# Kernel optimization log

Hardware: AMD Instinct MI355X
Metric: run time of the kernel (lower is better)

Reference implementation:

```python
import jax, jax.numpy as jnp
import numpy as np
from jax.scipy.stats import norm as jnorm

B, S, D, H, E, K, FF = 8, 256, 1024, 16, 4, 2, 4096
HD = D // H
NOISE_EPS = 0.01
LOSS_COEF = 0.01
EPS_FILL = float(np.finfo(float).eps)


def _ln(x, g, b):
    m = x.mean(-1, keepdims=True)
    v = x.var(-1, keepdims=True)
    return (x - m) * jax.lax.rsqrt(v + 1e-5) * g + b


def setup_inputs() -> dict:
    key = jax.random.key(0)
    ks = jax.random.split(key, 16)
    r = lambda i, shape, s=1.0: jax.random.normal(ks[i], shape, dtype=jnp.float32) * s
    return {
        "x": r(0, (B, S, D)),
        "e_outputs": r(1, (B, 64, D)),            # unused (is_lm=True) but part of signature
        "noise": r(2, (B, E)),                     # the randn_like(clean_logits) draw
        "w_gate": r(3, (D, E), 0.02),
        "w_noise": r(4, (D, E), 0.02),
        "Wq": r(5, (E, D, D), 0.02),
        "Wk": r(6, (E, D, D), 0.02),
        "Wv": r(7, (E, D, D), 0.02),
        "Wo": r(8, (E, D, D), 0.02),
        "W1": r(9, (E, D, FF), 0.02),
        "b1": jnp.zeros((E, FF), jnp.float32),
        "W2": r(10, (E, FF, D), 0.02),
        "b2": jnp.zeros((E, D), jnp.float32),
        "g1": jnp.ones((E, D), jnp.float32),
        "be1": jnp.zeros((E, D), jnp.float32),
        "g2": jnp.ones((E, D), jnp.float32),
        "be2": jnp.zeros((E, D), jnp.float32),
        "trg_mask": jnp.tril(jnp.ones((S, S), dtype=bool))[None, None],  # causal [1,1,S,S]
        "src_mask": jnp.ones((1, 1, 1, 64), dtype=bool),                 # unused (is_lm=True)
    }


def _cv_squared(v):
    # torch .var() is unbiased (ddof=1)
    return v.var(ddof=1) / (v.mean() ** 2 + 1e-10)


def reference(x, e_outputs, noise, w_gate, w_noise, Wq, Wk, Wv, Wo, W1, b1, W2, b2,
              g1, be1, g2, be2, trg_mask, src_mask):
    b, s, d = x.shape
    # ---- noisy top-k gating (per sample, on the sequence-sum) ----
    xs = x.sum(axis=1)                                   # [B, D]
    clean = xs @ w_gate                                  # [B, E]
    raw_noise = xs @ w_noise                             # [B, E]
    stddev = jax.nn.softplus(raw_noise) + NOISE_EPS      # train=True -> *1.0
    noisy = clean + noise * stddev                       # logits
    top_logits, top_idx = jax.lax.top_k(noisy, K + 1)    # [B, K+1]
    topk_gates = jax.nn.softmax(top_logits[:, :K], axis=1)
    gates = jnp.zeros_like(noisy).at[jnp.arange(b)[:, None], top_idx[:, :K]].set(topk_gates)
    # load: prob each expert's clean logit lands in the noisy top-k
    thr_in = top_logits[:, K:K + 1]                      # (k+1)-th noisy value
    thr_out = top_logits[:, K - 1:K]                     # k-th noisy value
    is_in = noisy > thr_in
    prob = jnp.where(is_in,
                     jnorm.cdf((clean - thr_in) / stddev),
                     jnorm.cdf((clean - thr_out) / stddev))
    load = prob.sum(0)                                   # [E]
    importance = gates.sum(0)                            # [E]
    loss = (_cv_squared(importance) + _cv_squared(load)) * LOSS_COEF

    # ---- experts: standard decoder layer (self-attn + FFN), is_lm -> no cross-attn ----
    neg = jnp.asarray(-1e9, x.dtype)
    scale = 1.0 / np.sqrt(HD)

    def expert(p):
        wq, wk, wv, wo, w1, bb1, w2, bb2, gg1, bbe1, gg2, bbe2 = p
        q = (x @ wq).reshape(b, s, H, HD)
        k_ = (x @ wk).reshape(b, s, H, HD)
        v = (x @ wv).reshape(b, s, H, HD)
        scores = jnp.einsum('bqhd,bkhd->bhqk', q, k_) * scale
        scores = jnp.where(trg_mask, scores, neg)
        attn = jax.nn.softmax(scores, axis=-1)
        o = jnp.einsum('bhqk,bkhd->bqhd', attn, v).reshape(b, s, d) @ wo
        h = _ln(x + o, gg1, bbe1)
        ff = jax.nn.relu(h @ w1 + bb1) @ w2 + bb2
        return _ln(h + ff, gg2, bbe2)

    outs = jax.vmap(expert)((Wq, Wk, Wv, Wo, W1, b1, W2, b2, g1, be1, g2, be2))  # [E,B,S,D]

    # ---- combine: scatter-add of gate-weighted expert outputs (dense equivalent) ----
    y = jnp.einsum('be,ebsd->bsd', gates, outs)
    y = jnp.where(y == 0, jnp.asarray(EPS_FILL, y.dtype), y)
    return y, loss
```

## Files before the change

### kernel.cpp

```cpp
#include <hip/hip_runtime.h>
#include <hip/hip_bf16.h>

typedef __bf16 bf16;
typedef __attribute__((ext_vector_type(4))) __bf16 bf16x4;
typedef __attribute__((ext_vector_type(8))) __bf16 bf16x8;
typedef __attribute__((ext_vector_type(4))) float floatx4;

constexpr int CB = 8, CS = 256, CD = 1024, CH = 16, CE = 4, CFF = 4096, CHD = 64;
constexpr long long DD  = 1048576;
constexpr long long DFF = 4194304;
constexpr long long BSD = 2097152;
constexpr long long PSD = 4194304;

constexpr size_t OFF_PART = 0;
constexpr size_t OFF_CLEAN= 262144;
constexpr size_t OFF_RAW  = 262272;
constexpr size_t OFF_GATES= 262400;
constexpr size_t OFF_EACT = 262528;
constexpr size_t OFF_PBE  = 262592;
constexpr size_t OFF_BP   = 262656;
constexpr size_t OFF_XBF  = 263168;
constexpr size_t OFF_WT   = OFF_XBF + (size_t)BSD*2;
constexpr size_t OFF_W1T  = OFF_WT  + (size_t)16*DD*2;
constexpr size_t OFF_W2T  = OFF_W1T + (size_t)4*DFF*2;
constexpr size_t OFF_QKV  = OFF_W2T + (size_t)4*DFF*2;
constexpr size_t OFF_AO   = OFF_QKV + (size_t)3*PSD*2;
constexpr size_t OFF_F1   = OFF_QKV;
constexpr size_t OFF_PB   = OFF_AO  + (size_t)PSD*2;
constexpr size_t OFF_VT   = OFF_PB;
constexpr size_t OFF_H    = OFF_PB  + (size_t)2*PSD*4;
constexpr size_t OFF_HBF  = OFF_H   + (size_t)PSD*4;

__global__ __launch_bounds__(256)
void cvt_xsum(const float* __restrict__ x, bf16* __restrict__ xbf, float* __restrict__ part) {
  int blk = blockIdx.x;
  int b = blk >> 3, ch = blk & 7;
  int t = threadIdx.x;
  float s0 = 0.f, s1 = 0.f, s2 = 0.f, s3 = 0.f;
  long long base4 = ((long long)(b*CS + ch*32))*CD / 4;
#pragma unroll 4
  for (int r = 0; r < 32; ++r) {
    long long i4 = base4 + (long long)r*(CD/4) + t;
    float4 v = ((const float4*)x)[i4];
    bf16x4 o; o[0] = (bf16)v.x; o[1] = (bf16)v.y; o[2] = (bf16)v.z; o[3] = (bf16)v.w;
    ((bf16x4*)xbf)[i4] = o;
    s0 += v.x; s1 += v.y; s2 += v.z; s3 += v.w;
  }
  float4 sv; sv.x = s0; sv.y = s1; sv.z = s2; sv.w = s3;
  ((float4*)(part + (long long)blk*CD))[t] = sv;
}

__global__ __launch_bounds__(256)
void gate_dots(const float* __restrict__ part, const float* __restrict__ wg,
               const float* __restrict__ wn, float* __restrict__ clean, float* __restrict__ raw) {
  int p = blockIdx.x, b = p >> 2, e = p & 3;
  int t = threadIdx.x;
  float s1 = 0.f, s2 = 0.f;
  for (int d = t; d < CD; d += 256) {
    float xv = 0.f;
#pragma unroll
    for (int c = 0; c < 8; ++c) xv += part[(long long)(b*8 + c)*CD + d];
    s1 += xv * wg[d*CE + e];
    s2 += xv * wn[d*CE + e];
  }
  for (int off = 32; off; off >>= 1) { s1 += __shfl_xor(s1, off); s2 += __shfl_xor(s2, off); }
  __shared__ float r1[4], r2[4];
  int lane = t & 63, w = t >> 6;
  if (lane == 0) { r1[w] = s1; r2[w] = s2; }
  __syncthreads();
  if (t == 0) { clean[p] = r1[0]+r1[1]+r1[2]+r1[3]; raw[p] = r2[0]+r2[1]+r2[2]+r2[3]; }
}

__global__ void gating_kernel(const float* __restrict__ clean, const float* __restrict__ raw,
                              const float* __restrict__ noise, float* __restrict__ gates,
                              int* __restrict__ eact, int* __restrict__ pairBE,
                              int* __restrict__ batchPair, float* __restrict__ loss_out) {
  if (threadIdx.x != 0) return;
  float imp[CE] = {0,0,0,0}, load[CE] = {0,0,0,0};
  int act[CE] = {0,0,0,0};
  for (int b = 0; b < CB; ++b) {
    float cl[CE], sd[CE], ny[CE];
    for (int e = 0; e < CE; ++e) {
      cl[e] = clean[b*CE + e];
      float rw = raw[b*CE + e];
      float sp = fmaxf(rw, 0.f) + log1pf(expf(-fabsf(rw)));
      sd[e] = sp + 0.01f;
      ny[e] = cl[e] + noise[b*CE + e]*sd[e];
    }
    int idx[CE] = {0,1,2,3};
    for (int a = 0; a < 3; ++a) {
      int best = a;
      for (int c = a + 1; c < 4; ++c) if (ny[idx[c]] > ny[idx[best]]) best = c;
      int tt = idx[a]; idx[a] = idx[best]; idx[best] = tt;
    }
    float l0 = ny[idx[0]], l1 = ny[idx[1]], l2 = ny[idx[2]];
    float e1 = expf(l1 - l0);
    float g0 = 1.f/(1.f + e1), g1v = e1/(1.f + e1);
    for (int e = 0; e < CE; ++e) gates[b*CE + e] = 0.f;
    gates[b*CE + idx[0]] = g0; gates[b*CE + idx[1]] = g1v;
    imp[idx[0]] += g0; imp[idx[1]] += g1v;
    act[idx[0]] = 1; act[idx[1]] = 1;
    for (int e = 0; e < CE; ++e) {
      bool is_in = ny[e] > l2;
      float thr = is_in ? l2 : l1;
      float zz = (cl[e] - thr) / sd[e];
      load[e] += 0.5f * erfcf(-zz * 0.70710678118654752440f);
    }
  }
  int pe2p[CB][CE];
  int pc = 0;
  for (int e = 0; e < CE; ++e)
    for (int b = 0; b < CB; ++b)
      if (gates[b*CE + e] != 0.f) { pairBE[pc] = b | (e << 8); pe2p[b][e] = pc; ++pc; }
  for (int b = 0; b < CB; ++b) {
    int s = 0;
    for (int e = 0; e < CE; ++e)
      if (gates[b*CE + e] != 0.f) batchPair[2*b + (s++)] = pe2p[b][e];
  }
  float m1 = 0.f, m2 = 0.f;
  for (int e = 0; e < CE; ++e) { m1 += imp[e]; m2 += load[e]; }
  m1 *= 0.25f; m2 *= 0.25f;
  float v1 = 0.f, v2 = 0.f;
  for (int e = 0; e < CE; ++e) { float d1 = imp[e]-m1, d2 = load[e]-m2; v1 += d1*d1; v2 += d2*d2; }
  v1 *= (1.f/3.f); v2 *= (1.f/3.f);
  loss_out[0] = 0.01f * (v1/(m1*m1 + 1e-10f) + v2/(m2*m2 + 1e-10f));
  for (int e = 0; e < CE; ++e) eact[e] = act[e];
}

__global__ __launch_bounds__(256)
void transcvt_all(const float* __restrict__ Wq, const float* __restrict__ Wk,
                  const float* __restrict__ Wv, const float* __restrict__ Wo,
                  const float* __restrict__ W1, const float* __restrict__ W2,
                  bf16* __restrict__ wT, bf16* __restrict__ w1T, bf16* __restrict__ w2T,
                  const int* __restrict__ eact) {
  int z = blockIdx.x;
  const float* src; bf16* d; int rows, cols, tk, tn, e;
  if (z < 4096) {
    int m = z >> 8, tt = z & 255; e = m >> 2; int which = m & 3;
    src = ((which == 0) ? Wq : (which == 1) ? Wk : (which == 2) ? Wv : Wo) + (long long)e*DD;
    d = wT + (long long)m*DD; rows = 1024; cols = 1024;
    tk = tt >> 4; tn = tt & 15;
  } else if (z < 8192) {
    int z2 = z - 4096; e = z2 >> 10; int tt = z2 & 1023;
    src = W1 + (long long)e*DFF; d = w1T + (long long)e*DFF;
    rows = 1024; cols = 4096; tk = tt >> 6; tn = tt & 63;
  } else {
    int z3 = z - 8192; e = z3 >> 10; int tt = z3 & 1023;
    src = W2 + (long long)e*DFF; d = w2T + (long long)e*DFF;
    rows = 4096; cols = 1024; tk = tt >> 4; tn = tt & 15;
  }
  if (eact[e] == 0) return;
  __shared__ float tile[64][65];
  int t = threadIdx.x;
  int k0 = tk*64, n0 = tn*64;
#pragma unroll
  for (int i = 0; i < 4; ++i) {
    int id = i*256 + t; int r = id >> 4, c4 = id & 15;
    float4 v = *(const float4*)&src[(long long)(k0 + r)*cols + n0 + c4*4];
    tile[r][c4*4 + 0] = v.x; tile[r][c4*4 + 1] = v.y;
    tile[r][c4*4 + 2] = v.z; tile[r][c4*4 + 3] = v.w;
  }
  __syncthreads();
#pragma unroll
  for (int i = 0; i < 2; ++i) {
    int id = i*256 + t; int n = id >> 3, ck = id & 7;
    bf16x8 o;
#pragma unroll
    for (int j = 0; j < 8; ++j) o[j] = (bf16)tile[ck*8 + j][n];
    *(bf16x8*)&d[(long long)(n0 + n)*rows + k0 + ck*8] = o;
  }
}

__global__ __launch_bounds__(256)
void transpose_v(const bf16* __restrict__ qkvC, bf16* __restrict__ vTb) {
  int z = blockIdx.z; int p = z >> 4, h = z & 15;
  const bf16* v = qkvC + 2*PSD + (long long)(p*CS)*CD + h*CHD;
  bf16* vt = vTb + (long long)(p*CH + h)*CHD*CS;
  __shared__ bf16 tile[32][33];
  int s0 = blockIdx.x*32, d0 = blockIdx.y*32;
  int tx = threadIdx.x % 32, ty = threadIdx.x / 32;
#pragma unroll
  for (int i = 0; i < 4; ++i)
    tile[ty + 8*i][tx] = v[(long long)(s0 + ty + 8*i)*CD + d0 + tx];
  __syncthreads();
#pragma unroll
  for (int i = 0; i < 4; ++i)
    vt[(long long)(d0 + ty + 8*i)*CS + s0 + tx] = tile[tx][ty + 8*i];
}

__device__ __forceinline__ void cp16(const bf16* g, bf16* l) {
  __builtin_amdgcn_global_load_lds((const __attribute__((address_space(1))) void*)g,
                                   (__attribute__((address_space(3))) void*)l, 16, 0, 0);
}

template<int R, int W>
__device__ __forceinline__ void stage(const bf16* __restrict__ src, int ld, bf16* dst) {
  constexpr int W8 = W/8;
  int t = threadIdx.x;
  int l = t & 63, wid = t >> 6;
#pragma unroll
  for (int i = 0; i < (R*W8)/256; ++i) {
    int idb = i*256 + wid*64;
    int id = idb + l;
    int row = id / W8, sl = id % W8;
    int gc = sl ^ (row & 7);
    cp16(src + (long long)row*ld + gc*8, dst + (long long)idb*8);
  }
}

__global__ __launch_bounds__(256)
void attn_fused(const bf16* __restrict__ qkvC, const bf16* __restrict__ vTb,
                bf16* __restrict__ aoC) {
  int h = blockIdx.x, p = blockIdx.y, qt = blockIdx.z;
  const bf16* qp = qkvC + (long long)(p*CS)*CD + h*CHD;
  const bf16* kp = qp + PSD;
  const bf16* vt = vTb + (long long)(p*CH + h)*CHD*CS;
  bf16* aop = aoC + (long long)(p*CS)*CD + h*CHD;

  __shared__ bf16 Ps[64*264];
  __shared__ float smaxL[64*4], ssumL[64*4], Lrow[64];

  int t = threadIdx.x, w = t >> 6, lane = t & 63, lr = lane & 15, quad = lane >> 4;

  floatx4 accs[4][4] = {};
  if (w <= qt) {
#pragma unroll
    for (int kk = 0; kk < 2; ++kk) {
      int c = kk*4 + quad;
      bf16x8 af[4], bfr[4];
#pragma unroll
      for (int i = 0; i < 4; ++i) {
        af[i]  = *(const bf16x8*)(qp + (long long)(qt*64 + i*16 + lr)*CD + c*8);
        bfr[i] = *(const bf16x8*)(kp + (long long)(w*64  + i*16 + lr)*CD + c*8);
      }
#pragma unroll
      for (int i = 0; i < 4; ++i)
#pragma unroll
        for (int j = 0; j < 4; ++j)
          accs[i][j] = __builtin_amdgcn_mfma_f32_16x16x32_bf16(af[i], bfr[j], accs[i][j], 0, 0, 0);
    }
  }
  float rmax[4][4];
#pragma unroll
  for (int i = 0; i < 4; ++i)
#pragma unroll
    for (int r = 0; r < 4; ++r) {
      int qrow = qt*64 + i*16 + quad*4 + r;
      float m = -3.0e38f;
#pragma unroll
      for (int j = 0; j < 4; ++j) {
        int kcol = w*64 + j*16 + lr;
        float s = accs[i][j][r]*0.125f;
        s = (kcol <= qrow) ? s : -3.0e38f;
        accs[i][j][r] = s;
        m = fmaxf(m, s);
      }
      rmax[i][r] = m;
    }
#pragma unroll
  for (int off = 1; off <= 8; off <<= 1)
#pragma unroll
    for (int i = 0; i < 4; ++i)
#pragma unroll
      for (int r = 0; r < 4; ++r) rmax[i][r] = fmaxf(rmax[i][r], __shfl_xor(rmax[i][r], off));
  if (lr == 0)
#pragma unroll
    for (int i = 0; i < 4; ++i)
#pragma unroll
      for (int r = 0; r < 4; ++r) smaxL[(i*16 + quad*4 + r)*4 + w] = rmax[i][r];
  __syncthreads();
  float rsum[4][4];
#pragma unroll
  for (int i = 0; i < 4; ++i)
#pragma unroll
    for (int r = 0; r < 4; ++r) {
      floatx4 mv = *(const floatx4*)&smaxL[(i*16 + quad*4 + r)*4];
      float M = fmaxf(fmaxf(mv[0], mv[1]), fmaxf(mv[2], mv[3]));
      float srow = 0.f;
#pragma unroll
      for (int j = 0; j < 4; ++j) {
        float pp = __expf(accs[i][j][r] - M);
        accs[i][j][r] = pp;
        srow += pp;
      }
      rsum[i][r] = srow;
    }
#pragma unroll
  for (int off = 1; off <= 8; off <<= 1)
#pragma unroll
    for (int i = 0; i < 4; ++i)
#pragma unroll
      for (int r = 0; r < 4; ++r) rsum[i][r] += __shfl_xor(rsum[i][r], off);
  if (lr == 0)
#pragma unroll
    for (int i = 0; i < 4; ++i)
#pragma unroll
      for (int r = 0; r < 4; ++r) ssumL[(i*16 + quad*4 + r)*4 + w] = rsum[i][r];
  __syncthreads();
  if (w == 0 && lr == 0) {
#pragma unroll
    for (int i = 0; i < 4; ++i)
#pragma unroll
      for (int r = 0; r < 4; ++r) {
        int m = i*16 + quad*4 + r;
        floatx4 sv = *(const floatx4*)&ssumL[m*4];
        Lrow[m] = sv[0] + sv[1] + sv[2] + sv[3];
      }
  }
  if (w <= qt) {
#pragma unroll
    for (int i = 0; i < 4; ++i)
#pragma unroll
      for (int j = 0; j < 4; ++j)
#pragma unroll
        for (int r = 0; r < 4; ++r)
          Ps[(i*16 + quad*4 + r)*264 + w*64 + j*16 + lr] = (bf16)accs[i][j][r];
  }
  __syncthreads();
  floatx4 acco[4] = {};
  int ksMax = (qt + 1)*2;
  for (int ks = 0; ks < ksMax; ++ks) {
    int c = ks*4 + quad;
    bf16x8 ap = *(const bf16x8*)(Ps + (w*16 + lr)*264 + c*8);
#pragma unroll
    for (int j = 0; j < 4; ++j) {
      bf16x8 bv = *(const bf16x8*)(vt + (long long)(j*16 + lr)*CS + c*8);
      acco[j] = __builtin_amdgcn_mfma_f32_16x16x32_bf16(ap, bv, acco[j], 0, 0, 0);
    }
  }
#pragma unroll
  for (int r = 0; r < 4; ++r) {
    int orow = w*16 + quad*4 + r;
    float inv = 1.f / Lrow[orow];
#pragma unroll
    for (int j = 0; j < 4; ++j)
      aop[(long long)(qt*64 + orow)*CD + j*16 + lr] = (bf16)(acco[j][r]*inv);
  }
}

__global__ __launch_bounds__(256)
void ln1_kernel(const float* __restrict__ x, const float* __restrict__ PbF,
                const float* __restrict__ gamma, const float* __restrict__ beta,
                float* __restrict__ h, bf16* __restrict__ hbf, const int* __restrict__ pairBE) {
  int row = blockIdx.x;
  int pbe = pairBE[row >> 8]; int pb = pbe & 255, pe = pbe >> 8;
  int t = threadIdx.x;
  float4 a = ((const float4*)(x + ((long long)pb*CS + (row & 255))*CD))[t];
  float4 b = ((const float4*)(PbF + (long long)row*CD))[t];
  float4 c = ((const float4*)(PbF + PSD + (long long)row*CD))[t];
  float v0 = a.x + b.x + c.x, v1 = a.y + b.y + c.y;
  float v2 = a.z + b.z + c.z, v3 = a.w + b.w + c.w;
  float s  = v0 + v1 + v2 + v3;
  float s2 = v0*v0 + v1*v1 + v2*v2 + v3*v3;
  int lane = t & 63, wave = t >> 6;
  for (int off = 32; off; off >>= 1) { s += __shfl_xor(s, off); s2 += __shfl_xor(s2, off); }
  __shared__ float red[8];
  if (lane == 0) { red[wave*2] = s; red[wave*2 + 1] = s2; }
  __syncthreads();
  s  = red[0] + red[2] + red[4] + red[6];
  s2 = red[1] + red[3] + red[5] + red[7];
  float mean = s * (1.f/CD);
  float rstd = rsqrtf(s2*(1.f/CD) - mean*mean + 1e-5f);
  float4 gm = ((const float4*)(gamma + (long long)pe*CD))[t];
  float4 bt = ((const float4*)(beta  + (long long)pe*CD))[t];
  float4 o;
  o.x = (v0 - mean)*rstd*gm.x + bt.x;
  o.y = (v1 - mean)*rstd*gm.y + bt.y;
  o.z = (v2 - mean)*rstd*gm.z + bt.z;
  o.w = (v3 - mean)*rstd*gm.w + bt.w;
  ((float4*)(h + (long long)row*CD))[t] = o;
  bf16x4 ob; ob[0] = (bf16)o.x; ob[1] = (bf16)o.y; ob[2] = (bf16)o.z; ob[3] = (bf16)o.w;
  ((bf16x4*)(hbf + (long long)row*CD))[t] = ob;
}

__global__ __launch_bounds__(256)
void ln2y_kernel(const float* __restrict__ h, const bf16* __restrict__ PbB,
                 const float* __restrict__ gamma, const float* __restrict__ beta,
                 float* __restrict__ y, const float* __restrict__ gates,
                 const int* __restrict__ pairBE, const int* __restrict__ batchPair) {
  int row = blockIdx.x;
  int b = row >> 8, sIdx = row & 255;
  int p0 = batchPair[2*b], p1 = batchPair[2*b + 1];
  int e0 = pairBE[p0] >> 8, e1 = pairBE[p1] >> 8;
  float gv0 = gates[b*CE + e0], gv1 = gates[b*CE + e1];
  long long r0 = (long long)p0*CS + sIdx, r1 = (long long)p1*CS + sIdx;
  int t = threadIdx.x;
  float4 a = ((const float4*)(h + r0*CD))[t];
  float4 c = ((const float4*)(h + r1*CD))[t];
#pragma unroll
  for (int k = 0; k < 4; ++k) {
    bf16x4 pa = ((const bf16x4*)(PbB + (long long)k*PSD + r0*CD))[t];
    bf16x4 pc = ((const bf16x4*)(PbB + (long long)k*PSD + r1*CD))[t];
    a.x += (float)pa[0]; a.y += (float)pa[1]; a.z += (float)pa[2]; a.w += (float)pa[3];
    c.x += (float)pc[0]; c.y += (float)pc[1]; c.z += (float)pc[2]; c.w += (float)pc[3];
  }
  float sA = a.x + a.y + a.z + a.w;
  float sA2 = a.x*a.x + a.y*a.y + a.z*a.z + a.w*a.w;
  float sB = c.x + c.y + c.z + c.w;
  float sB2 = c.x*c.x + c.y*c.y + c.z*c.z + c.w*c.w;
  int lane = t & 63, wave = t >> 6;
  for (int off = 32; off; off >>= 1) {
    sA += __shfl_xor(sA, off); sA2 += __shfl_xor(sA2, off);
    sB += __shfl_xor(sB, off); sB2 += __shfl_xor(sB2, off);
  }
  __shared__ float red[16];
  if (lane == 0) { red[wave*4] = sA; red[wave*4+1] = sA2; red[wave*4+2] = sB; red[wave*4+3] = sB2; }
  __syncthreads();
  sA  = red[0] + red[4] + red[8]  + red[12];
  sA2 = red[1] + red[5] + red[9]  + red[13];
  sB  = red[2] + red[6] + red[10] + red[14];
  sB2 = red[3] + red[7] + red[11] + red[15];
  float mA = sA*(1.f/CD), mB = sB*(1.f/CD);
  float rsA = rsqrtf(sA2*(1.f/CD) - mA*mA + 1e-5f);
  float rsB = rsqrtf(sB2*(1.f/CD) - mB*mB + 1e-5f);
  float4 gm0 = ((const float4*)(gamma + (long long)e0*CD))[t];
  float4 bt0 = ((const float4*)(beta  + (long long)e0*CD))[t];
  float4 gm1 = ((const float4*)(gamma + (long long)e1*CD))[t];
  float4 bt1 = ((const float4*)(beta  + (long long)e1*CD))[t];
  float4 o;
  o.x = gv0*((a.x - mA)*rsA*gm0.x + bt0.x) + gv1*((c.x - mB)*rsB*gm1.x + bt1.x);
  o.y = gv0*((a.y - mA)*rsA*gm0.y + bt0.y) + gv1*((c.y - mB)*rsB*gm1.y + bt1.y);
  o.z = gv0*((a.z - mA)*rsA*gm0.z + bt0.z) + gv1*((c.z - mB)*rsB*gm1.z + bt1.z);
  o.w = gv0*((a.w - mA)*rsA*gm0.w + bt0.w) + gv1*((c.w - mB)*rsB*gm1.w + bt1.w);
  constexpr float EF = 2.2204460492503131e-16f;
  o.x = (o.x == 0.f) ? EF : o.x;  o.y = (o.y == 0.f) ? EF : o.y;
  o.z = (o.z == 0.f) ? EF : o.z;  o.w = (o.w == 0.f) ? EF : o.w;
  ((float4*)(y + (long long)row*CD))[t] = o;
}

enum { EPI_BF16 = 0, EPI_F32 = 1, EPI_BRELU = 2, EPI_BIASBF16 = 3 };

template<int EPI, int KS, bool A_BATCH>
__global__ __launch_bounds__(256)
void gemm_nt(const bf16* __restrict__ A, const bf16* __restrict__ Bt, void* __restrict__ Cv,
             int K , int lda, int ldb, int ldc,
             long long oBe, long long oBmat, long long oCmat, long long oCk,
             const float* __restrict__ bias, long long biasStride,
             const int* __restrict__ pairBE) {
  constexpr int BM = 128, BN = 128;
  int z = blockIdx.z;
  int zk = z % KS, mat = z / KS;
  int m0 = blockIdx.x * BM, n0 = blockIdx.y * BN;
  int pbe = pairBE[m0 >> 8]; int pb = pbe & 255, pe = pbe >> 8;
  const bf16* Ab = A + (A_BATCH ? ((long long)pb*CS + (m0 & 255))*lda : (long long)m0*lda)
                     + (long long)zk*K;
  const bf16* Bb = Bt + (long long)pe*oBe + (long long)mat*oBmat + (long long)zk*K
                      + (long long)n0*ldb;
  long long coff = (long long)mat*oCmat + (long long)zk*oCk;

  __shared__ bf16 As[BM*64];
  __shared__ bf16 Bs[BN*64];

  int wave = threadIdx.x >> 6;
  int lane = threadIdx.x & 63;
  int wm = wave >> 1, wn = wave & 1;
  int lr = lane & 15;
  int quad = lane >> 4;

  floatx4 acc[4][4] = {};

  for (int kt = 0; kt < K; kt += 64) {
    stage<BM, 64>(Ab + kt, lda, As);
    stage<BN, 64>(Bb + kt, ldb, Bs);
    __syncthreads();
#pragma unroll
    for (int kk = 0; kk < 2; ++kk) {
      bf16x8 af[4], bfr[4];
#pragma unroll
      for (int i = 0; i < 4; ++i) {
        int c = kk*4 + quad;
        int m = wm*64 + i*16 + lr;
        af[i]  = *(const bf16x8*)(As + m*64 + ((c ^ (m & 7))*8));
        int n = wn*64 + i*16 + lr;
        bfr[i] = *(const bf16x8*)(Bs + n*64 + ((c ^ (n & 7))*8));
      }
#pragma unroll
      for (int i = 0; i < 4; ++i)
#pragma unroll
        for (int j = 0; j < 4; ++j)
          acc[i][j] = __builtin_amdgcn_mfma_f32_16x16x32_bf16(af[i], bfr[j], acc[i][j], 0, 0, 0);
    }
    __syncthreads();
  }

#pragma unroll
  for (int j = 0; j < 4; ++j) {
    int col = n0 + wn*64 + j*16 + lr;
    float bv = 0.f;
    if constexpr (EPI == EPI_BRELU || EPI == EPI_BIASBF16)
      if (zk == 0) bv = bias[(long long)pe*biasStride + col];
#pragma unroll
    for (int i = 0; i < 4; ++i) {
#pragma unroll
      for (int r = 0; r < 4; ++r) {
        int row = m0 + wm*64 + i*16 + quad*4 + r;
        float v = acc[i][j][r] + bv;
        long long idx = coff + (long long)row*ldc + col;
        if constexpr (EPI == EPI_BF16)          ((bf16*)Cv)[idx] = (bf16)v;
        else if constexpr (EPI == EPI_F32)      ((float*)Cv)[idx] = v;
        else if constexpr (EPI == EPI_BRELU)    ((bf16*)Cv)[idx] = (bf16)fmaxf(v, 0.f);
        else                                    ((bf16*)Cv)[idx] = (bf16)v;
      }
    }
  }
}

extern "C" void kernel_launch(void* const* d_in, const int* in_sizes, int n_in,
                              void* d_out, int out_size, void* d_ws, size_t ws_size,
                              hipStream_t stream) {
  const float* x       = (const float*)d_in[0];
  const float* noise   = (const float*)d_in[2];
  const float* w_gate  = (const float*)d_in[3];
  const float* w_noise = (const float*)d_in[4];
  const float* Wq      = (const float*)d_in[5];
  const float* Wk      = (const float*)d_in[6];
  const float* Wv      = (const float*)d_in[7];
  const float* Wo      = (const float*)d_in[8];
  const float* W1      = (const float*)d_in[9];
  const float* b1      = (const float*)d_in[10];
  const float* W2      = (const float*)d_in[11];
  const float* b2      = (const float*)d_in[12];
  const float* g1      = (const float*)d_in[13];
  const float* be1     = (const float*)d_in[14];
  const float* g2      = (const float*)d_in[15];
  const float* be2     = (const float*)d_in[16];

  char* ws = (char*)d_ws;
  float* y    = (float*)d_out;
  float* loss = y + (size_t)BSD;

  float* part  = (float*)(ws + OFF_PART);
  float* clean = (float*)(ws + OFF_CLEAN);
  float* raw   = (float*)(ws + OFF_RAW);
  float* gates = (float*)(ws + OFF_GATES);
  int*   eact  = (int*)  (ws + OFF_EACT);
  int*   pairBE= (int*)  (ws + OFF_PBE);
  int*   batchPair = (int*)(ws + OFF_BP);
  bf16*  xbf   = (bf16*) (ws + OFF_XBF);
  bf16*  wT    = (bf16*) (ws + OFF_WT);
  bf16*  w1T   = (bf16*) (ws + OFF_W1T);
  bf16*  w2T   = (bf16*) (ws + OFF_W2T);
  bf16*  qkvC  = (bf16*) (ws + OFF_QKV);
  bf16*  aoC   = (bf16*) (ws + OFF_AO);
  bf16*  f1    = (bf16*) (ws + OFF_F1);
  bf16*  vTb   = (bf16*) (ws + OFF_VT);
  float* PbF   = (float*)(ws + OFF_PB);
  bf16*  PbB   = (bf16*) (ws + OFF_PB);
  float* h     = (float*)(ws + OFF_H);
  bf16*  hbf   = (bf16*) (ws + OFF_HBF);

  cvt_xsum<<<64, 256, 0, stream>>>(x, xbf, part);
  gate_dots<<<32, 256, 0, stream>>>(part, w_gate, w_noise, clean, raw);
  gating_kernel<<<1, 64, 0, stream>>>(clean, raw, noise, gates, eact, pairBE, batchPair, loss);
  transcvt_all<<<12288, 256, 0, stream>>>(Wq, Wk, Wv, Wo, W1, W2, wT, w1T, w2T, eact);

  gemm_nt<EPI_BF16, 1, true><<<dim3(32, 8, 3), 256, 0, stream>>>(
      xbf, wT, qkvC, 1024, 1024, 1024, 1024,
      4*DD, DD, PSD, 0, nullptr, 0, pairBE);

  transpose_v<<<dim3(8, 2, 256), 256, 0, stream>>>(qkvC, vTb);

  attn_fused<<<dim3(CH, 16, 4), 256, 0, stream>>>(qkvC, vTb, aoC);

  gemm_nt<EPI_F32, 2, false><<<dim3(32, 8, 2), 256, 0, stream>>>(
      aoC, wT + 3*DD, PbF, 512, 1024, 1024, 1024,
      4*DD, 0, 0, PSD, nullptr, 0, pairBE);

  ln1_kernel<<<4096, 256, 0, stream>>>(x, PbF, g1, be1, h, hbf, pairBE);

  gemm_nt<EPI_BRELU, 1, false><<<dim3(32, 32, 1), 256, 0, stream>>>(
      hbf, w1T, f1, 1024, 1024, 1024, 4096,
      DFF, 0, 0, 0, b1, CFF, pairBE);

  gemm_nt<EPI_BIASBF16, 4, false><<<dim3(32, 8, 4), 256, 0, stream>>>(
      f1, w2T, PbB, 1024, 4096, 4096, 1024,
      DFF, 0, 0, PSD, b2, CD, pairBE);

  ln2y_kernel<<<2048, 256, 0, stream>>>(h, PbB, g2, be2, y, gates, pairBE, batchPair);
}
```

Measured before the change: 520.1 us.

## Fuse fp32 weight transpose-convert into GEMM B-tile staging

Removes the separate transcvt_all pass that transposed and converted all expert weights to bf16 in workspace. The GEMMs now read the original fp32 weights directly and convert them to bf16 while staging the B tile into shared memory. This avoids a full write and re-read of the converted weights, but each GEMM block now issues strided scalar fp32 loads instead of async 16-byte global-to-LDS copies. Weight tiles reused across M-blocks are also re-converted in every block.

```diff
diff --git a/kernel.cpp b/kernel.cpp
--- a/kernel.cpp
+++ b/kernel.cpp
@@ -20,10 +20,7 @@
 constexpr size_t OFF_PBE  = 262592;
 constexpr size_t OFF_BP   = 262656;
 constexpr size_t OFF_XBF  = 263168;
-constexpr size_t OFF_WT   = OFF_XBF + (size_t)BSD*2;
-constexpr size_t OFF_W1T  = OFF_WT  + (size_t)16*DD*2;
-constexpr size_t OFF_W2T  = OFF_W1T + (size_t)4*DFF*2;
-constexpr size_t OFF_QKV  = OFF_W2T + (size_t)4*DFF*2;
+constexpr size_t OFF_QKV  = OFF_XBF + (size_t)BSD*2;
 constexpr size_t OFF_AO   = OFF_QKV + (size_t)3*PSD*2;
 constexpr size_t OFF_F1   = OFF_QKV;
 constexpr size_t OFF_PB   = OFF_AO  + (size_t)PSD*2;
@@ -128,50 +125,6 @@
 }
 
 __global__ __launch_bounds__(256)
-void transcvt_all(const float* __restrict__ Wq, const float* __restrict__ Wk,
-                  const float* __restrict__ Wv, const float* __restrict__ Wo,
-                  const float* __restrict__ W1, const float* __restrict__ W2,
-                  bf16* __restrict__ wT, bf16* __restrict__ w1T, bf16* __restrict__ w2T,
-                  const int* __restrict__ eact) {
-  int z = blockIdx.x;
-  const float* src; bf16* d; int rows, cols, tk, tn, e;
-  if (z < 4096) {
-    int m = z >> 8, tt = z & 255; e = m >> 2; int which = m & 3;
-    src = ((which == 0) ? Wq : (which == 1) ? Wk : (which == 2) ? Wv : Wo) + (long long)e*DD;
-    d = wT + (long long)m*DD; rows = 1024; cols = 1024;
-    tk = tt >> 4; tn = tt & 15;
-  } else if (z < 8192) {
-    int z2 = z - 4096; e = z2 >> 10; int tt = z2 & 1023;
-    src = W1 + (long long)e*DFF; d = w1T + (long long)e*DFF;
-    rows = 1024; cols = 4096; tk = tt >> 6; tn = tt & 63;
-  } else {
-    int z3 = z - 8192; e = z3 >> 10; int tt = z3 & 1023;
-    src = W2 + (long long)e*DFF; d = w2T + (long long)e*DFF;
-    rows = 4096; cols = 1024; tk = tt >> 4; tn = tt & 15;
-  }
-  if (eact[e] == 0) return;
-  __shared__ float tile[64][65];
-  int t = threadIdx.x;
-  int k0 = tk*64, n0 = tn*64;
-#pragma unroll
-  for (int i = 0; i < 4; ++i) {
-    int id = i*256 + t; int r = id >> 4, c4 = id & 15;
-    float4 v = *(const float4*)&src[(long long)(k0 + r)*cols + n0 + c4*4];
-    tile[r][c4*4 + 0] = v.x; tile[r][c4*4 + 1] = v.y;
-    tile[r][c4*4 + 2] = v.z; tile[r][c4*4 + 3] = v.w;
-  }
-  __syncthreads();
-#pragma unroll
-  for (int i = 0; i < 2; ++i) {
-    int id = i*256 + t; int n = id >> 3, ck = id & 7;
-    bf16x8 o;
-#pragma unroll
-    for (int j = 0; j < 8; ++j) o[j] = (bf16)tile[ck*8 + j][n];
-    *(bf16x8*)&d[(long long)(n0 + n)*rows + k0 + ck*8] = o;
-  }
-}
-
-__global__ __launch_bounds__(256)
 void transpose_v(const bf16* __restrict__ qkvC, bf16* __restrict__ vTb) {
   int z = blockIdx.z; int p = z >> 4, h = z & 15;
   const bf16* v = qkvC + 2*PSD + (long long)(p*CS)*CD + h*CHD;
@@ -205,6 +158,25 @@
     int row = id / W8, sl = id % W8;
     int gc = sl ^ (row & 7);
     cp16(src + (long long)row*ld + gc*8, dst + (long long)idb*8);
+  }
+}
+
+__device__ __forceinline__ void stageBf32(const float* __restrict__ src, int ld, bf16* Bs) {
+  int t = threadIdx.x;
+  int l = t & 63, w = t >> 6;
+  int n = (w & 1)*64 + l;
+  int cbase = (w >> 1)*4;
+  const float* col = src + n;
+#pragma unroll
+  for (int cc = 0; cc < 4; ++cc) {
+    int c = cbase + cc;
+    float f[8];
+#pragma unroll
+    for (int j = 0; j < 8; ++j) f[j] = col[(long long)(c*8 + j)*ld];
+    bf16x8 o;
+#pragma unroll
+    for (int j = 0; j < 8; ++j) o[j] = (bf16)f[j];
+    *(bf16x8*)(Bs + n*64 + ((c ^ (n & 7))*8)) = o;
   }
 }
 
@@ -432,9 +404,11 @@
 
 template<int EPI, int KS, bool A_BATCH>
 __global__ __launch_bounds__(256)
-void gemm_nt(const bf16* __restrict__ A, const bf16* __restrict__ Bt, void* __restrict__ Cv,
+void gemm_nt(const bf16* __restrict__ A, const float* __restrict__ B0,
+             const float* __restrict__ B1, const float* __restrict__ B2,
+             void* __restrict__ Cv,
              int K , int lda, int ldb, int ldc,
-             long long oBe, long long oBmat, long long oCmat, long long oCk,
+             long long oBe, long long oCmat, long long oCk,
              const float* __restrict__ bias, long long biasStride,
              const int* __restrict__ pairBE) {
   constexpr int BM = 128, BN = 128;
@@ -444,8 +418,8 @@
   int pbe = pairBE[m0 >> 8]; int pb = pbe & 255, pe = pbe >> 8;
   const bf16* Ab = A + (A_BATCH ? ((long long)pb*CS + (m0 & 255))*lda : (long long)m0*lda)
                      + (long long)zk*K;
-  const bf16* Bb = Bt + (long long)pe*oBe + (long long)mat*oBmat + (long long)zk*K
-                      + (long long)n0*ldb;
+  const float* Wsel = (mat == 0) ? B0 : (mat == 1) ? B1 : B2;
+  const float* Bb = Wsel + (long long)pe*oBe + (long long)zk*K*ldb + n0;
   long long coff = (long long)mat*oCmat + (long long)zk*oCk;
 
   __shared__ bf16 As[BM*64];
@@ -461,7 +435,7 @@
 
   for (int kt = 0; kt < K; kt += 64) {
     stage<BM, 64>(Ab + kt, lda, As);
-    stage<BN, 64>(Bb + kt, ldb, Bs);
+    stageBf32(Bb + (long long)kt*ldb, ldb, Bs);
     __syncthreads();
 #pragma unroll
     for (int kk = 0; kk < 2; ++kk) {
@@ -537,9 +511,6 @@
   int*   pairBE= (int*)  (ws + OFF_PBE);
   int*   batchPair = (int*)(ws + OFF_BP);
   bf16*  xbf   = (bf16*) (ws + OFF_XBF);
-  bf16*  wT    = (bf16*) (ws + OFF_WT);
-  bf16*  w1T   = (bf16*) (ws + OFF_W1T);
-  bf16*  w2T   = (bf16*) (ws + OFF_W2T);
   bf16*  qkvC  = (bf16*) (ws + OFF_QKV);
   bf16*  aoC   = (bf16*) (ws + OFF_AO);
   bf16*  f1    = (bf16*) (ws + OFF_F1);
@@ -552,29 +523,28 @@
   cvt_xsum<<<64, 256, 0, stream>>>(x, xbf, part);
   gate_dots<<<32, 256, 0, stream>>>(part, w_gate, w_noise, clean, raw);
   gating_kernel<<<1, 64, 0, stream>>>(clean, raw, noise, gates, eact, pairBE, batchPair, loss);
-  transcvt_all<<<12288, 256, 0, stream>>>(Wq, Wk, Wv, Wo, W1, W2, wT, w1T, w2T, eact);
 
   gemm_nt<EPI_BF16, 1, true><<<dim3(32, 8, 3), 256, 0, stream>>>(
-      xbf, wT, qkvC, 1024, 1024, 1024, 1024,
-      4*DD, DD, PSD, 0, nullptr, 0, pairBE);
+      xbf, Wq, Wk, Wv, qkvC, 1024, 1024, 1024, 1024,
+      DD, PSD, 0, nullptr, 0, pairBE);
 
   transpose_v<<<dim3(8, 2, 256), 256, 0, stream>>>(qkvC, vTb);
 
   attn_fused<<<dim3(CH, 16, 4), 256, 0, stream>>>(qkvC, vTb, aoC);
 
   gemm_nt<EPI_F32, 2, false><<<dim3(32, 8, 2), 256, 0, stream>>>(
-      aoC, wT + 3*DD, PbF, 512, 1024, 1024, 1024,
-      4*DD, 0, 0, PSD, nullptr, 0, pairBE);
+      aoC, Wo, Wo, Wo, PbF, 512, 1024, 1024, 1024,
+      DD, 0, PSD, nullptr, 0, pairBE);
 
   ln1_kernel<<<4096, 256, 0, stream>>>(x, PbF, g1, be1, h, hbf, pairBE);
 
   gemm_nt<EPI_BRELU, 1, false><<<dim3(32, 32, 1), 256, 0, stream>>>(
-      hbf, w1T, f1, 1024, 1024, 1024, 4096,
-      DFF, 0, 0, 0, b1, CFF, pairBE);
+      hbf, W1, W1, W1, f1, 1024, 1024, 4096, 4096,
+      DFF, 0, 0, b1, CFF, pairBE);
 
   gemm_nt<EPI_BIASBF16, 4, false><<<dim3(32, 8, 4), 256, 0, stream>>>(
-      f1, w2T, PbB, 1024, 4096, 4096, 1024,
-      DFF, 0, 0, PSD, b2, CD, pairBE);
+      f1, W2, W2, W2, PbB, 1024, 4096, 1024, 1024,
+      DFF, 0, PSD, b2, CD, pairBE);
 
   ln2y_kernel<<<2048, 256, 0, stream>>>(h, PbB, g2, be2, y, gates, pairBE, batchPair);
 }
```

After: 553.1 us. 6.3% more time.

## Transpose weights in registers per wave and remap GEMM workgroups for XCD locality

Applied to the files above, without the earlier changes.

The weight transpose/convert kernel now gives each 64x64 tile to a single wave, which loads an 8x8 float sub-block per lane into registers and writes transposed bf16x8 vectors directly, with no shared-memory tile or barrier. This is meant to cut LDS traffic and synchronisation in the kernel that moves the most bytes. The GEMM also remaps its linear workgroup index so that consecutive blocks on the same XCD cover contiguous tiles, aiming for better L2 reuse. The cost is less coalesced global reads, since each lane reads 32-byte pieces from 8 rows, and the remap assumes the workgroup count divides by 8.

```diff
diff --git a/kernel.cpp b/kernel.cpp
--- a/kernel.cpp
+++ b/kernel.cpp
@@ -128,12 +128,12 @@
 }
 
 __global__ __launch_bounds__(256)
-void transcvt_all(const float* __restrict__ Wq, const float* __restrict__ Wk,
-                  const float* __restrict__ Wv, const float* __restrict__ Wo,
-                  const float* __restrict__ W1, const float* __restrict__ W2,
-                  bf16* __restrict__ wT, bf16* __restrict__ w1T, bf16* __restrict__ w2T,
-                  const int* __restrict__ eact) {
-  int z = blockIdx.x;
+void wtrans_reg(const float* __restrict__ Wq, const float* __restrict__ Wk,
+                const float* __restrict__ Wv, const float* __restrict__ Wo,
+                const float* __restrict__ W1, const float* __restrict__ W2,
+                bf16* __restrict__ wT, bf16* __restrict__ w1T, bf16* __restrict__ w2T,
+                const int* __restrict__ eact) {
+  int z = blockIdx.x*4 + (threadIdx.x >> 6);
   const float* src; bf16* d; int rows, cols, tk, tn, e;
   if (z < 4096) {
     int m = z >> 8, tt = z & 255; e = m >> 2; int which = m & 3;
@@ -150,24 +150,26 @@
     rows = 4096; cols = 1024; tk = tt >> 4; tn = tt & 15;
   }
   if (eact[e] == 0) return;
-  __shared__ float tile[64][65];
-  int t = threadIdx.x;
+  int lane = threadIdx.x & 63;
+  int ln = lane >> 3, lk = lane & 7;
   int k0 = tk*64, n0 = tn*64;
-#pragma unroll
-  for (int i = 0; i < 4; ++i) {
-    int id = i*256 + t; int r = id >> 4, c4 = id & 15;
-    float4 v = *(const float4*)&src[(long long)(k0 + r)*cols + n0 + c4*4];
-    tile[r][c4*4 + 0] = v.x; tile[r][c4*4 + 1] = v.y;
-    tile[r][c4*4 + 2] = v.z; tile[r][c4*4 + 3] = v.w;
-  }
-  __syncthreads();
-#pragma unroll
-  for (int i = 0; i < 2; ++i) {
-    int id = i*256 + t; int n = id >> 3, ck = id & 7;
+  const float* s = src + (long long)(k0 + lk*8)*cols + n0 + ln*8;
+  float4 f[8][2];
+#pragma unroll
+  for (int j = 0; j < 8; ++j) {
+    f[j][0] = *(const float4*)(s + (long long)j*cols);
+    f[j][1] = *(const float4*)(s + (long long)j*cols + 4);
+  }
+  bf16* dp = d + (long long)(n0 + ln*8)*rows + k0 + lk*8;
+#pragma unroll
+  for (int jn = 0; jn < 8; ++jn) {
     bf16x8 o;
 #pragma unroll
-    for (int j = 0; j < 8; ++j) o[j] = (bf16)tile[ck*8 + j][n];
-    *(bf16x8*)&d[(long long)(n0 + n)*rows + k0 + ck*8] = o;
+    for (int jk = 0; jk < 8; ++jk) {
+      const float* fp = (const float*)&f[jk][jn >> 2];
+      o[jk] = (bf16)fp[jn & 3];
+    }
+    *(bf16x8*)(dp + (long long)jn*rows) = o;
   }
 }
 
@@ -440,7 +442,11 @@
   constexpr int BM = 128, BN = 128;
   int z = blockIdx.z;
   int zk = z % KS, mat = z / KS;
-  int m0 = blockIdx.x * BM, n0 = blockIdx.y * BN;
+  int gx = gridDim.x;
+  int nwg = gx * gridDim.y;
+  int lin = blockIdx.x + gx*blockIdx.y;
+  int nl  = (lin & 7)*(nwg >> 3) + (lin >> 3);
+  int m0 = (nl % gx) * BM, n0 = (nl / gx) * BN;
   int pbe = pairBE[m0 >> 8]; int pb = pbe & 255, pe = pbe >> 8;
   const bf16* Ab = A + (A_BATCH ? ((long long)pb*CS + (m0 & 255))*lda : (long long)m0*lda)
                      + (long long)zk*K;
@@ -552,7 +558,7 @@
   cvt_xsum<<<64, 256, 0, stream>>>(x, xbf, part);
   gate_dots<<<32, 256, 0, stream>>>(part, w_gate, w_noise, clean, raw);
   gating_kernel<<<1, 64, 0, stream>>>(clean, raw, noise, gates, eact, pairBE, batchPair, loss);
-  transcvt_all<<<12288, 256, 0, stream>>>(Wq, Wk, Wv, Wo, W1, W2, wT, w1T, w2T, eact);
+  wtrans_reg<<<3072, 256, 0, stream>>>(Wq, Wk, Wv, Wo, W1, W2, wT, w1T, w2T, eact);
 
   gemm_nt<EPI_BF16, 1, true><<<dim3(32, 8, 3), 256, 0, stream>>>(
       xbf, wT, qkvC, 1024, 1024, 1024, 1024,
```

After: 505.8 us. 1.03x faster.
